# Performance work log

Hardware: AMD Instinct MI355X
Metric: run time of the kernel (lower is better)

Reference implementation:

```python
import jax, jax.numpy as jnp
import numpy as np
import math

E, H, T, B = 1024, 16, 2048, 2
HD = E // H  # 64
NUM_BUCKETS, MAX_DIST = 32, 128


def setup_inputs() -> dict:
    key = jax.random.key(0)
    ks = jax.random.split(key, 8)
    s = 0.02
    return {
        'query': jax.random.normal(ks[0], (T, B, E), jnp.float32),
        'q_w': jax.random.normal(ks[1], (E, E), jnp.float32) * s,
        'q_b': jnp.zeros((E,), jnp.float32),
        'k_w': jax.random.normal(ks[2], (E, E), jnp.float32) * s,
        'k_b': jnp.zeros((E,), jnp.float32),
        'v_w': jax.random.normal(ks[3], (E, E), jnp.float32) * s,
        'v_b': jnp.zeros((E,), jnp.float32),
        'out_w': jax.random.normal(ks[4], (E, E), jnp.float32) * s,
        'out_b': jnp.zeros((E,), jnp.float32),
        'rel_emb': jax.random.normal(ks[5], (NUM_BUCKETS, H), jnp.float32) * s,
        'grep_w': jax.random.normal(ks[6], (8, HD), jnp.float32) * s,
        'grep_b': jnp.zeros((8,), jnp.float32),
        'grep_a': jnp.ones((1, H, 1, 1), jnp.float32),
    }


def _rel_bucket(rp):
    # bidirectional T5-style bucketing, num_buckets=32 -> nb=16, max_exact=8
    nb = NUM_BUCKETS // 2
    buckets = (rp > 0).astype(jnp.int32) * nb
    rpa = jnp.abs(rp)
    max_exact = nb // 2
    large = max_exact + (
        jnp.log(jnp.maximum(rpa, 1).astype(jnp.float32) / max_exact)
        / math.log(MAX_DIST / max_exact) * (nb - max_exact)
    ).astype(jnp.int32)
    large = jnp.minimum(large, nb - 1)
    return buckets + jnp.where(rpa < max_exact, rpa, large)


def reference(query, q_w, q_b, k_w, k_b, v_w, v_b, out_w, out_b, rel_emb, grep_w, grep_b, grep_a):
    t, b, e = query.shape
    scaling = HD ** -0.5
    # relative-position bucket bias -> [H, T, T]
    rp = jnp.arange(t)[None, :] - jnp.arange(t)[:, None]  # memory - context
    pos_bias = jnp.transpose(rel_emb[_rel_bucket(rp)], (2, 0, 1))  # [H,T,T]
    # GRU-style gate computed from the RAW query (pre q_proj)
    ql = jnp.transpose(query, (1, 0, 2)).reshape(b, t, H, HD).transpose(0, 2, 1, 3)  # [B,H,T,HD]
    gate_in = (ql @ grep_w.T + grep_b).reshape(b, H, t, 2, 4).sum(-1)  # [B,H,T,2]
    gate = jax.nn.sigmoid(gate_in)
    gate_a, gate_b = gate[..., 0:1], gate[..., 1:2]  # each [B,H,T,1]
    gate_a_1 = gate_a * (gate_b * grep_a - 1.0) + 2.0  # [B,H,T,1]
    bias = gate_a_1 * pos_bias[None]  # [B,H,T,T]
    # projections (self-attention: key = value = query)
    q = (query @ q_w.T + q_b) * scaling
    k = query @ k_w.T + k_b
    v = query @ v_w.T + v_b
    qh = q.reshape(t, b, H, HD)
    kh = k.reshape(t, b, H, HD)
    vh = v.reshape(t, b, H, HD)
    scores = jnp.einsum('tbhd,sbhd->bhts', qh, kh) + bias
    attn = jax.nn.softmax(scores, axis=-1)
    out = jnp.einsum('bhts,sbhd->tbhd', attn, vh).reshape(t, b, e)
    return out @ out_w.T + out_b
```

## Files before the change

### kernel.cpp

```cpp
#include <hip/hip_runtime.h>
#include <math.h>

typedef unsigned short u16;
typedef unsigned int u32;
typedef __bf16 bf16x8 __attribute__((ext_vector_type(8)));
typedef float f32x4 __attribute__((ext_vector_type(4)));
typedef float f32x16 __attribute__((ext_vector_type(16)));

__device__ __forceinline__ u32 f2bf(float f) {
  union { float f; u32 u; } v; v.f = f;
  u32 r = v.u + 0x7fffu + ((v.u >> 16) & 1u);
  return r >> 16;
}

__device__ __forceinline__ u32 pkbf(float a, float b) {
  u32 r;
  asm("v_cvt_pk_bf16_f32 %0, %1, %2" : "=v"(r) : "v"(a), "v"(b));
  return r;
}

__device__ __forceinline__ float ex2(float x) {
  float r;
  asm("v_exp_f32 %0, %1" : "=v"(r) : "v"(x));
  return r;
}

__device__ __forceinline__ void gld16(const void* g, void* s) {
  __builtin_amdgcn_global_load_lds(
      reinterpret_cast<__attribute__((address_space(1))) u32*>((size_t)g),
      reinterpret_cast<__attribute__((address_space(3))) u32*>((u32)(size_t)s),
      16, 0, 0);
}

__global__ __launch_bounds__(256) void prepk(
    const float* __restrict__ query, const float* __restrict__ q_w,
    const float* __restrict__ k_w, const float* __restrict__ v_w,
    const float* __restrict__ out_w, const float* __restrict__ rel_emb,
    const float* __restrict__ grep_w, const float* __restrict__ grep_b,
    const float* __restrict__ grep_a,
    u16* __restrict__ qbf, u16* __restrict__ wqb, u16* __restrict__ wkb,
    u16* __restrict__ wvb, u16* __restrict__ wob,
    float* __restrict__ lut, float* __restrict__ gate) {
  const int bid = blockIdx.x, tid = threadIdx.x;
  if (bid < 8192) {
    const float* src; u16* dst; int i0;
    if (bid < 4096)      { src = query; dst = qbf; i0 = bid; }
    else if (bid < 5120) { src = q_w;   dst = wqb; i0 = bid - 4096; }
    else if (bid < 6144) { src = k_w;   dst = wkb; i0 = bid - 5120; }
    else if (bid < 7168) { src = v_w;   dst = wvb; i0 = bid - 6144; }
    else                 { src = out_w; dst = wob; i0 = bid - 7168; }
    const int i = i0 * 256 + tid;
    float4 v = ((const float4*)src)[i];
    uint2 o;
    o.x = f2bf(v.x) | (f2bf(v.y) << 16);
    o.y = f2bf(v.z) | (f2bf(v.w) << 16);
    ((uint2*)dst)[i] = o;
  } else if (bid < 8208) {
    const int dix = (bid - 8192) * 256 + tid;
    int rp = dix - 2048;
    int bucket = (rp > 0) ? 16 : 0;
    int rpa = rp < 0 ? -rp : rp;
    if (rpa < 8) {
      bucket += rpa;
    } else {
      int large = 8 + (int)(logf((float)rpa * 0.125f) * (8.0f / 2.772588722239781f));
      bucket += (large < 15) ? large : 15;
    }
    const float LOG2E = 1.4426950408889634f;
#pragma unroll
    for (int h = 0; h < 16; ++h) lut[h * 4096 + dix] = rel_emb[bucket * 16 + h] * LOG2E;
  } else {
    __shared__ __align__(16) float gw[8][64];
    __shared__ float gb[8];
    __shared__ float ga[16];
    if (tid < 128) ((float4*)&gw[0][0])[tid] = ((const float4*)grep_w)[tid];
    if (tid < 8) gb[tid] = grep_b[tid];
    if (tid < 16) ga[tid] = grep_a[tid];
    __syncthreads();
    const int i = (bid - 8208) * 256 + tid;
    const int t = i & 2047, h = (i >> 11) & 15, b = i >> 15;
    const float* x = query + ((size_t)t * 2 + b) * 1024 + h * 64;
    float acc[8] = {0, 0, 0, 0, 0, 0, 0, 0};
    for (int e4 = 0; e4 < 16; ++e4) {
      float4 xv = ((const float4*)x)[e4];
#pragma unroll
      for (int j = 0; j < 8; ++j)
        acc[j] += xv.x * gw[j][e4 * 4] + xv.y * gw[j][e4 * 4 + 1] +
                  xv.z * gw[j][e4 * 4 + 2] + xv.w * gw[j][e4 * 4 + 3];
    }
    float sA = acc[0] + acc[1] + acc[2] + acc[3] + gb[0] + gb[1] + gb[2] + gb[3];
    float sB = acc[4] + acc[5] + acc[6] + acc[7] + gb[4] + gb[5] + gb[6] + gb[7];
    float gA = 1.0f / (1.0f + expf(-sA));
    float gB = 1.0f / (1.0f + expf(-sB));
    gate[i] = gA * (gB * ga[h] - 1.0f) + 2.0f;
  }
}

__global__ __launch_bounds__(256) void gemmk(
    const u16* __restrict__ A,
    const u16* __restrict__ W0, const u16* __restrict__ W1, const u16* __restrict__ W2,
    const float* __restrict__ b0, const float* __restrict__ b1, const float* __restrict__ b2,
    u16* __restrict__ qa, u16* __restrict__ kst, u16* __restrict__ vst,
    float* __restrict__ fout, int moBase) {
  const int mode = moBase + (int)blockIdx.z;
  const u16* W = (mode == 1) ? W1 : (mode == 2) ? W2 : W0;
  const float* bias = (mode == 1) ? b1 : (mode == 2) ? b2 : b0;

  __shared__ __align__(16) u16 As[64 * 64];
  __shared__ __align__(16) u16 Bs[128 * 64];

  const int tid = threadIdx.x;
  const int l = tid & 63;
  const int w = tid >> 6;
  const int wr = w >> 1, wc = w & 1;
  const int m0 = blockIdx.y * 64, n0 = blockIdx.x * 128;
  const int li = l >> 3, ls = l & 7;

  f32x4 acc[2][4] = {};

  for (int k0 = 0; k0 < 1024; k0 += 64) {
#pragma unroll
    for (int j = 0; j < 2; ++j) {
      const int rr = w * 16 + j * 8 + li;
      const int cs = ls ^ (rr & 7);
      gld16(A + ((size_t)(m0 + rr) << 10) + k0 + cs * 8, &As[(w * 16 + j * 8) * 64]);
    }
#pragma unroll
    for (int j = 0; j < 4; ++j) {
      const int rr = w * 32 + j * 8 + li;
      const int cs = ls ^ (rr & 7);
      gld16(W + ((size_t)(n0 + rr) << 10) + k0 + cs * 8, &Bs[(w * 32 + j * 8) * 64]);
    }
    __syncthreads();
#pragma unroll
    for (int ks = 0; ks < 2; ++ks) {
      bf16x8 af[2], bfr[4];
#pragma unroll
      for (int mf = 0; mf < 2; ++mf) {
        const int row = wr * 32 + mf * 16 + (l & 15);
        const int slot = (ks * 4 + (l >> 4)) ^ (row & 7);
        af[mf] = *(const bf16x8*)&As[row * 64 + slot * 8];
      }
#pragma unroll
      for (int nf = 0; nf < 4; ++nf) {
        const int row = wc * 64 + nf * 16 + (l & 15);
        const int slot = (ks * 4 + (l >> 4)) ^ (row & 7);
        bfr[nf] = *(const bf16x8*)&Bs[row * 64 + slot * 8];
      }
#pragma unroll
      for (int mf = 0; mf < 2; ++mf)
#pragma unroll
        for (int nf = 0; nf < 4; ++nf)
          acc[mf][nf] = __builtin_amdgcn_mfma_f32_16x16x32_bf16(af[mf], bfr[nf], acc[mf][nf], 0, 0, 0);
    }
    __syncthreads();
  }

  const float QSC = 0.125f * 1.4426950408889634f;
#pragma unroll
  for (int mf = 0; mf < 2; ++mf)
#pragma unroll
    for (int nf = 0; nf < 4; ++nf)
#pragma unroll
      for (int r = 0; r < 4; ++r) {
        const int row = m0 + wr * 32 + mf * 16 + (l >> 4) * 4 + r;
        const int col = n0 + wc * 64 + nf * 16 + (l & 15);
        float v = acc[mf][nf][r] + bias[col];
        const int t = row >> 1, bb = row & 1, hh = col >> 6, d = col & 63;
        const size_t bh = (size_t)bb * 16 + hh;
        if (mode == 0) {
          v *= QSC;
          qa[((bh * 2048 + t) << 6) + d] = (u16)f2bf(v);
        } else if (mode == 1) {
          kst[((bh * 64 + (t >> 5)) << 11) + ((d >> 3) << 8) + ((t & 31) << 3) + (d & 7)] = (u16)f2bf(v);
        } else if (mode == 2) {
          vst[((bh * 64 + (t >> 5)) << 11) + (((t >> 3) & 3) << 9) + (d << 3) + (t & 7)] = (u16)f2bf(v);
        } else {
          fout[((size_t)row << 10) + col] = v;
        }
      }
}

__global__ __launch_bounds__(256, 4) void flashk(const u16* __restrict__ qa,
                                                 const u16* __restrict__ kst,
                                                 const u16* __restrict__ vst,
                                                 const float* __restrict__ lutg,
                                                 const float* __restrict__ gatew,
                                                 u16* __restrict__ aout) {
  const int B = blockIdx.x;
  const int xcd = B & 7, j = B >> 3;
  const int bh = xcd * 4 + (j >> 5);
  const int qt = j & 31;
  const int hh = bh & 15, b = bh >> 4;
  const int tid = threadIdx.x, l = tid & 63, w = tid >> 6;
  const int half = w >> 1, sub = w & 1;
  const int hi = l >> 5, q = l & 31;
  const int q0b = qt * 64;
  const int q0w = q0b + sub * 32;
  const int qg = q0w + q;

  __shared__ union {
    struct { u16 K[2][2][2048]; u16 V[2][2][2048]; } m;
    struct { float pm[4][32]; float pl[4][32]; float pO[4][32][68]; } c;
  } S;
  __shared__ __align__(16) float slice[288];

  for (int i = tid; i < 288; i += 256) slice[i] = lutg[hh * 4096 + 1920 + i];

  const size_t tb0 = (size_t)bh * 64;
  const u16* Q = qa + ((size_t)bh << 17);

  bf16x8 qf[4];
#pragma unroll
  for (int mk = 0; mk < 4; ++mk)
    qf[mk] = *(const bf16x8*)&Q[((size_t)qg << 6) + mk * 16 + hi * 8];

  const float g = gatew[((size_t)bh << 11) + qg];
  const float gcm = g * lutg[hh * 4096];
  const float gcp = g * lutg[hh * 4096 + 4095];

  float m_run = -3e38f, l_run = 0.0f;
  f32x16 oacc[2] = {};

  {
    const u16* kt0 = kst + ((tb0 + half * 32) << 11) + l * 8;
    const u16* vt0 = vst + ((tb0 + half * 32) << 11) + l * 8;
    if (sub == 0) {
#pragma unroll
      for (int i = 0; i < 4; ++i) gld16(kt0 + i * 512, &S.m.K[half][0][i * 512]);
    } else {
#pragma unroll
      for (int i = 0; i < 4; ++i) gld16(vt0 + i * 512, &S.m.V[half][0][i * 512]);
    }
  }
  __syncthreads();

  for (int ts = 0; ts < 32; ++ts) {
    const int bf_ = ts & 1;
    if (ts < 31) {
      const u16* ktn = kst + ((tb0 + half * 32 + ts + 1) << 11) + l * 8;
      const u16* vtn = vst + ((tb0 + half * 32 + ts + 1) << 11) + l * 8;
      if (sub == 0) {
#pragma unroll
        for (int i = 0; i < 4; ++i) gld16(ktn + i * 512, &S.m.K[half][bf_ ^ 1][i * 512]);
      } else {
#pragma unroll
        for (int i = 0; i < 4; ++i) gld16(vtn + i * 512, &S.m.V[half][bf_ ^ 1][i * 512]);
      }
    }
    const u16* Kb = &S.m.K[half][bf_][0];
    const u16* Vb = &S.m.V[half][bf_][0];
    const int s0 = half * 1024 + ts * 32;

    f32x16 s = {};
#pragma unroll
    for (int mk = 0; mk < 4; ++mk) {
      bf16x8 kf = *(const bf16x8*)&Kb[(mk * 2 + hi) * 256 + q * 8];
      s = __builtin_amdgcn_mfma_f32_32x32x16_bf16(kf, qf[mk], s, 0, 0, 0);
    }

    const int kt = (s0 - q0w) >> 5;
    const bool far = (kt <= -4) | (kt >= 4);
    float gc = 0.0f;
    float mx;
    if (far) {
      gc = (kt < 0) ? gcm : gcp;
      float t0_ = fmaxf(fmaxf(s[0], s[1]), s[2]);
      float t1_ = fmaxf(fmaxf(s[3], s[4]), s[5]);
      float t2_ = fmaxf(fmaxf(s[6], s[7]), s[8]);
      float t3_ = fmaxf(fmaxf(s[9], s[10]), s[11]);
      float t4_ = fmaxf(fmaxf(s[12], s[13]), s[14]);
      mx = fmaxf(fmaxf(fmaxf(t0_, t1_), t2_), fmaxf(fmaxf(t3_, t4_), s[15]));
      mx = fmaxf(mx, __shfl_xor(mx, 32, 64)) + gc;
    } else {
      const int sb = s0 - q0w + 128 + 4 * hi - q;
#pragma unroll
      for (int reg = 0; reg < 16; ++reg) {
        const int kloc = (reg & 3) + 8 * (reg >> 2);
        s[reg] = fmaf(g, slice[sb + kloc], s[reg]);
      }
      float t0_ = fmaxf(fmaxf(s[0], s[1]), s[2]);
      float t1_ = fmaxf(fmaxf(s[3], s[4]), s[5]);
      float t2_ = fmaxf(fmaxf(s[6], s[7]), s[8]);
      float t3_ = fmaxf(fmaxf(s[9], s[10]), s[11]);
      float t4_ = fmaxf(fmaxf(s[12], s[13]), s[14]);
      mx = fmaxf(fmaxf(fmaxf(t0_, t1_), t2_), fmaxf(fmaxf(t3_, t4_), s[15]));
      mx = fmaxf(mx, __shfl_xor(mx, 32, 64));
    }
    if (!__all(mx - m_run <= 11.5f)) {
      const float mnew = fmaxf(m_run, mx);
      const float sc = ex2(m_run - mnew);
      l_run *= sc;
#pragma unroll
      for (int r = 0; r < 16; ++r) { oacc[0][r] *= sc; oacc[1][r] *= sc; }
      m_run = mnew;
    }
    const float mref = m_run - gc;
#pragma unroll
    for (int reg = 0; reg < 16; ++reg) s[reg] = ex2(s[reg] - mref);
    {
      float r0 = (s[0] + s[1]) + (s[2] + s[3]);
      float r1 = (s[4] + s[5]) + (s[6] + s[7]);
      float r2 = (s[8] + s[9]) + (s[10] + s[11]);
      float r3 = (s[12] + s[13]) + (s[14] + s[15]);
      float rsum = (r0 + r1) + (r2 + r3);
      rsum += __shfl_xor(rsum, 32, 64);
      l_run += rsum;
    }
    bf16x8 pa[2];
#pragma unroll
    for (int kh = 0; kh < 2; ++kh) {
      const int rb = kh * 8;
      const u32 X0 = pkbf(s[rb + 0], s[rb + 1]);
      const u32 X1 = pkbf(s[rb + 2], s[rb + 3]);
      const u32 Y0 = pkbf(s[rb + 4], s[rb + 5]);
      const u32 Y1 = pkbf(s[rb + 6], s[rb + 7]);
      const u32 E0 = hi ? X0 : Y0;
      const u32 E1 = hi ? X1 : Y1;
      const u32 Ep0 = (u32)__shfl_xor((int)E0, 32, 64);
      const u32 Ep1 = (u32)__shfl_xor((int)E1, 32, 64);
      union { u32 wds[4]; bf16x8 v; } pu;
      pu.wds[0] = hi ? Ep0 : X0;
      pu.wds[1] = hi ? Ep1 : X1;
      pu.wds[2] = hi ? Y0 : Ep0;
      pu.wds[3] = hi ? Y1 : Ep1;
      pa[kh] = pu.v;
    }
#pragma unroll
    for (int dt = 0; dt < 2; ++dt)
#pragma unroll
      for (int kh = 0; kh < 2; ++kh) {
        bf16x8 vf = *(const bf16x8*)&Vb[(kh * 2 + hi) * 512 + dt * 256 + q * 8];
        oacc[dt] = __builtin_amdgcn_mfma_f32_32x32x16_bf16(vf, pa[kh], oacc[dt], 0, 0, 0);
      }
    __syncthreads();
  }

  __syncthreads();
  if (hi == 0) { S.c.pm[w][q] = m_run; S.c.pl[w][q] = l_run; }
#pragma unroll
  for (int dt = 0; dt < 2; ++dt)
#pragma unroll
    for (int g4 = 0; g4 < 4; ++g4) {
      float4 v4;
      v4.x = oacc[dt][g4 * 4 + 0];
      v4.y = oacc[dt][g4 * 4 + 1];
      v4.z = oacc[dt][g4 * 4 + 2];
      v4.w = oacc[dt][g4 * 4 + 3];
      *(float4*)&S.c.pO[w][q][dt * 32 + g4 * 8 + hi * 4] = v4;
    }
  __syncthreads();

  const int rr = tid >> 2;
  const int dc = (tid & 3) << 4;
  const int rl = rr & 31, sr = rr >> 5;
  const float mA = S.c.pm[sr][rl], mB = S.c.pm[2 + sr][rl];
  const float M = fmaxf(mA, mB);
  const float eA = ex2(mA - M), eB = ex2(mB - M);
  const float inv = 1.0f / (S.c.pl[sr][rl] * eA + S.c.pl[2 + sr][rl] * eB);
  union { u16 hb[16]; uint4 u4[2]; } st;
#pragma unroll
  for (int c4 = 0; c4 < 4; ++c4) {
    const float4 a = *(const float4*)&S.c.pO[sr][rl][dc + c4 * 4];
    const float4 bb = *(const float4*)&S.c.pO[2 + sr][rl][dc + c4 * 4];
    st.hb[c4 * 4 + 0] = (u16)f2bf((a.x * eA + bb.x * eB) * inv);
    st.hb[c4 * 4 + 1] = (u16)f2bf((a.y * eA + bb.y * eB) * inv);
    st.hb[c4 * 4 + 2] = (u16)f2bf((a.z * eA + bb.z * eB) * inv);
    st.hb[c4 * 4 + 3] = (u16)f2bf((a.w * eA + bb.w * eB) * inv);
  }
  u16* dst = &aout[(((size_t)(q0b + rr) * 2 + b) << 10) + hh * 64 + dc];
  *(uint4*)dst = st.u4[0];
  *(uint4*)(dst + 8) = st.u4[1];
}

extern "C" void kernel_launch(void* const* d_in, const int* in_sizes, int n_in,
                              void* d_out, int out_size, void* d_ws, size_t ws_size,
                              hipStream_t stream) {
  (void)in_sizes; (void)n_in; (void)out_size; (void)ws_size;
  const float* query  = (const float*)d_in[0];
  const float* q_w    = (const float*)d_in[1];
  const float* q_b    = (const float*)d_in[2];
  const float* k_w    = (const float*)d_in[3];
  const float* k_b    = (const float*)d_in[4];
  const float* v_w    = (const float*)d_in[5];
  const float* v_b    = (const float*)d_in[6];
  const float* out_w  = (const float*)d_in[7];
  const float* out_b  = (const float*)d_in[8];
  const float* rel_emb= (const float*)d_in[9];
  const float* grep_w = (const float*)d_in[10];
  const float* grep_b = (const float*)d_in[11];
  const float* grep_a = (const float*)d_in[12];

  char* ws = (char*)d_ws;
  const size_t MB = 1ull << 20;
  u16* qbf  = (u16*)(ws + 0 * MB);
  u16* wqb  = (u16*)(ws + 8 * MB);
  u16* wkb  = (u16*)(ws + 10 * MB);
  u16* wvb  = (u16*)(ws + 12 * MB);
  u16* wob  = (u16*)(ws + 14 * MB);
  u16* qav  = (u16*)(ws + 16 * MB);
  u16* kstg = (u16*)(ws + 24 * MB);
  u16* vstg = (u16*)(ws + 32 * MB);
  u16* aout = (u16*)(ws + 40 * MB);
  float* lut  = (float*)(ws + 48 * MB);
  float* gate = (float*)(ws + 48 * MB + 256 * 1024);

  prepk<<<dim3(8464), 256, 0, stream>>>(query, q_w, k_w, v_w, out_w, rel_emb,
                                        grep_w, grep_b, grep_a,
                                        qbf, wqb, wkb, wvb, wob, lut, gate);

  gemmk<<<dim3(8, 64, 3), 256, 0, stream>>>(qbf, wqb, wkb, wvb, q_b, k_b, v_b,
                                            qav, kstg, vstg, nullptr, 0);
  flashk<<<dim3(1024), 256, 0, stream>>>(qav, kstg, vstg, lut, gate, aout);
  gemmk<<<dim3(8, 64, 1), 256, 0, stream>>>(aout, wob, nullptr, nullptr, out_b, nullptr, nullptr,
                                            nullptr, nullptr, nullptr, (float*)d_out, 3);
}
```

Measured before the change: 146.7 us.

## Fuse Q/K/V projections into one GEMM sharing the A tile across three weights

The GEMM kernel becomes a template that computes NM weight matrices per block. The QKV launch now loads each A tile once and multiplies it against Q, K and V weight tiles of 64 columns each, where before each mode ran as a separate 128-column block. This cuts redundant A-tile loads. The output projection now uses 64x64 tiles, which doubles its grid and may lower per-block reuse. The fused block uses more accumulator registers and shared memory, which could reduce occupancy.

```diff
diff --git a/kernel.cpp b/kernel.cpp
--- a/kernel.cpp
+++ b/kernel.cpp
@@ -96,27 +96,26 @@
   }
 }
 
+template <int MB, int NM>
 __global__ __launch_bounds__(256) void gemmk(
     const u16* __restrict__ A,
     const u16* __restrict__ W0, const u16* __restrict__ W1, const u16* __restrict__ W2,
     const float* __restrict__ b0, const float* __restrict__ b1, const float* __restrict__ b2,
     u16* __restrict__ qa, u16* __restrict__ kst, u16* __restrict__ vst,
-    float* __restrict__ fout, int moBase) {
-  const int mode = moBase + (int)blockIdx.z;
-  const u16* W = (mode == 1) ? W1 : (mode == 2) ? W2 : W0;
-  const float* bias = (mode == 1) ? b1 : (mode == 2) ? b2 : b0;
-
+    float* __restrict__ fout) {
   __shared__ __align__(16) u16 As[64 * 64];
-  __shared__ __align__(16) u16 Bs[128 * 64];
+  __shared__ __align__(16) u16 Bs[NM][64 * 64];
 
   const int tid = threadIdx.x;
   const int l = tid & 63;
   const int w = tid >> 6;
   const int wr = w >> 1, wc = w & 1;
-  const int m0 = blockIdx.y * 64, n0 = blockIdx.x * 128;
+  const int m0 = blockIdx.y * 64, n0 = blockIdx.x * 64;
   const int li = l >> 3, ls = l & 7;
-
-  f32x4 acc[2][4] = {};
+  const u16* const Ws[3] = {W0, W1, W2};
+  const float* const bs[3] = {b0, b1, b2};
+
+  f32x4 acc[NM][2][2] = {};
 
   for (int k0 = 0; k0 < 1024; k0 += 64) {
 #pragma unroll
@@ -124,17 +123,14 @@
       const int rr = w * 16 + j * 8 + li;
       const int cs = ls ^ (rr & 7);
       gld16(A + ((size_t)(m0 + rr) << 10) + k0 + cs * 8, &As[(w * 16 + j * 8) * 64]);
-    }
-#pragma unroll
-    for (int j = 0; j < 4; ++j) {
-      const int rr = w * 32 + j * 8 + li;
-      const int cs = ls ^ (rr & 7);
-      gld16(W + ((size_t)(n0 + rr) << 10) + k0 + cs * 8, &Bs[(w * 32 + j * 8) * 64]);
+#pragma unroll
+      for (int mm = 0; mm < NM; ++mm)
+        gld16(Ws[mm] + ((size_t)(n0 + rr) << 10) + k0 + cs * 8, &Bs[mm][(w * 16 + j * 8) * 64]);
     }
     __syncthreads();
 #pragma unroll
     for (int ks = 0; ks < 2; ++ks) {
-      bf16x8 af[2], bfr[4];
+      bf16x8 af[2];
 #pragma unroll
       for (int mf = 0; mf < 2; ++mf) {
         const int row = wr * 32 + mf * 16 + (l & 15);
@@ -142,43 +138,52 @@
         af[mf] = *(const bf16x8*)&As[row * 64 + slot * 8];
       }
 #pragma unroll
-      for (int nf = 0; nf < 4; ++nf) {
-        const int row = wc * 64 + nf * 16 + (l & 15);
-        const int slot = (ks * 4 + (l >> 4)) ^ (row & 7);
-        bfr[nf] = *(const bf16x8*)&Bs[row * 64 + slot * 8];
+      for (int mm = 0; mm < NM; ++mm) {
+        bf16x8 bfr[2];
+#pragma unroll
+        for (int nf = 0; nf < 2; ++nf) {
+          const int row = wc * 32 + nf * 16 + (l & 15);
+          const int slot = (ks * 4 + (l >> 4)) ^ (row & 7);
+          bfr[nf] = *(const bf16x8*)&Bs[mm][row * 64 + slot * 8];
+        }
+#pragma unroll
+        for (int mf = 0; mf < 2; ++mf)
+#pragma unroll
+          for (int nf = 0; nf < 2; ++nf)
+            acc[mm][mf][nf] = __builtin_amdgcn_mfma_f32_16x16x32_bf16(af[mf], bfr[nf], acc[mm][mf][nf], 0, 0, 0);
       }
-#pragma unroll
-      for (int mf = 0; mf < 2; ++mf)
-#pragma unroll
-        for (int nf = 0; nf < 4; ++nf)
-          acc[mf][nf] = __builtin_amdgcn_mfma_f32_16x16x32_bf16(af[mf], bfr[nf], acc[mf][nf], 0, 0, 0);
     }
     __syncthreads();
   }
 
   const float QSC = 0.125f * 1.4426950408889634f;
 #pragma unroll
-  for (int mf = 0; mf < 2; ++mf)
-#pragma unroll
-    for (int nf = 0; nf < 4; ++nf)
-#pragma unroll
-      for (int r = 0; r < 4; ++r) {
-        const int row = m0 + wr * 32 + mf * 16 + (l >> 4) * 4 + r;
-        const int col = n0 + wc * 64 + nf * 16 + (l & 15);
-        float v = acc[mf][nf][r] + bias[col];
-        const int t = row >> 1, bb = row & 1, hh = col >> 6, d = col & 63;
-        const size_t bh = (size_t)bb * 16 + hh;
-        if (mode == 0) {
-          v *= QSC;
-          qa[((bh * 2048 + t) << 6) + d] = (u16)f2bf(v);
-        } else if (mode == 1) {
-          kst[((bh * 64 + (t >> 5)) << 11) + ((d >> 3) << 8) + ((t & 31) << 3) + (d & 7)] = (u16)f2bf(v);
-        } else if (mode == 2) {
-          vst[((bh * 64 + (t >> 5)) << 11) + (((t >> 3) & 3) << 9) + (d << 3) + (t & 7)] = (u16)f2bf(v);
-        } else {
-          fout[((size_t)row << 10) + col] = v;
+  for (int mm = 0; mm < NM; ++mm) {
+    const int mode = MB + mm;
+    const float* bias = bs[mm];
+#pragma unroll
+    for (int mf = 0; mf < 2; ++mf)
+#pragma unroll
+      for (int nf = 0; nf < 2; ++nf)
+#pragma unroll
+        for (int r = 0; r < 4; ++r) {
+          const int row = m0 + wr * 32 + mf * 16 + (l >> 4) * 4 + r;
+          const int col = n0 + wc * 32 + nf * 16 + (l & 15);
+          float v = acc[mm][mf][nf][r] + bias[col];
+          const int t = row >> 1, bb = row & 1, hh = col >> 6, d = col & 63;
+          const size_t bh = (size_t)bb * 16 + hh;
+          if (mode == 0) {
+            v *= QSC;
+            qa[((bh * 2048 + t) << 6) + d] = (u16)f2bf(v);
+          } else if (mode == 1) {
+            kst[((bh * 64 + (t >> 5)) << 11) + ((d >> 3) << 8) + ((t & 31) << 3) + (d & 7)] = (u16)f2bf(v);
+          } else if (mode == 2) {
+            vst[((bh * 64 + (t >> 5)) << 11) + (((t >> 3) & 3) << 9) + (d << 3) + (t & 7)] = (u16)f2bf(v);
+          } else {
+            fout[((size_t)row << 10) + col] = v;
+          }
         }
-      }
+  }
 }
 
 __global__ __launch_bounds__(256, 4) void flashk(const u16* __restrict__ qa,
@@ -409,9 +414,9 @@
                                         grep_w, grep_b, grep_a,
                                         qbf, wqb, wkb, wvb, wob, lut, gate);
 
-  gemmk<<<dim3(8, 64, 3), 256, 0, stream>>>(qbf, wqb, wkb, wvb, q_b, k_b, v_b,
-                                            qav, kstg, vstg, nullptr, 0);
+  gemmk<0, 3><<<dim3(16, 64), 256, 0, stream>>>(qbf, wqb, wkb, wvb, q_b, k_b, v_b,
+                                                qav, kstg, vstg, nullptr);
   flashk<<<dim3(1024), 256, 0, stream>>>(qav, kstg, vstg, lut, gate, aout);
-  gemmk<<<dim3(8, 64, 1), 256, 0, stream>>>(aout, wob, nullptr, nullptr, out_b, nullptr, nullptr,
-                                            nullptr, nullptr, nullptr, (float*)d_out, 3);
-}
+  gemmk<3, 1><<<dim3(16, 64), 256, 0, stream>>>(aout, wob, wob, wob, out_b, out_b, out_b,
+                                                nullptr, nullptr, nullptr, (float*)d_out);
+}
```

After: 143.1 us. 2.4% less time.
